# Performance work log

Measured on AMD Instinct MI355X. Metric: run time of the kernel, lower is better.

Reference implementation:

```python
import jax, jax.numpy as jnp
import numpy as np
from jax import lax

BETA = 0.95     # snn.Leaky(0.95)
THRESH = 1.0    # snntorch default threshold
ALPHA = 2.0     # snntorch ATan surrogate default alpha
NUM_STEPS = 100

@jax.custom_vjp
def spike_fn(u):
    return (u > 0).astype(u.dtype)

def _spike_fwd(u):
    return (u > 0).astype(u.dtype), u

def _spike_bwd(u, g):
    surr = (ALPHA / 2.0) / (1.0 + (jnp.pi / 2.0 * ALPHA * u) ** 2)
    return (g * surr,)

spike_fn.defvjp(_spike_fwd, _spike_bwd)

def leaky_scan(inputs, mem0):
    # inputs: [T, ...]; snntorch Leaky with reset_mechanism='zero'
    def step(carry, x_t):
        mem, _ = carry
        reset = spike_fn(mem - THRESH)       # spike detected from previous mem
        base = BETA * mem + x_t
        mem = base - reset * base            # zero-reset
        spk = spike_fn(mem - THRESH)
        return (mem, spk), None
    (mem, spk), _ = lax.scan(step, (mem0, jnp.zeros_like(mem0)), inputs)
    return spk, mem

def setup_inputs():
    key = jax.random.key(0)
    ks = jax.random.split(key, 7)
    B, T, W, C = 32, 2000, 512, 4
    H, O = 1024, 10
    s = lambda n: 1.0 / np.sqrt(n)
    return {
        "x": jax.random.normal(ks[0], (B, T, W, C), jnp.float32),
        "conv_w": jax.random.uniform(ks[1], (C,), jnp.float32, -s(C), s(C)),
        "conv_b": jax.random.uniform(ks[2], (), jnp.float32, -s(C), s(C)),
        "hidden_w": jax.random.uniform(ks[3], (H, W), jnp.float32, -s(W), s(W)),
        "hidden_b": jax.random.uniform(ks[4], (H,), jnp.float32, -s(W), s(W)),
        "out_w": jax.random.uniform(ks[5], (O, H), jnp.float32, -s(H), s(H)),
        "out_b": jax.random.uniform(ks[6], (O,), jnp.float32, -s(H), s(H)),
    }

def reference(x, conv_w, conv_b, hidden_w, hidden_b, out_w, out_b):
    B, T, W, _ = x.shape
    # 1x1 conv fusing 4 antenna channels: (B,T,W,4)->(B,T,W)
    fused = jnp.einsum('bhwc,c->bhw', x, conv_w) + conv_b
    G = T // NUM_STEPS
    fused = fused.reshape(B, G, NUM_STEPS, W)      # [B,G,S,W]
    seq1 = jnp.moveaxis(fused, 2, 0)               # [S,B,G,W] time-major
    spk, _ = leaky_scan(seq1, jnp.zeros((B, G, W), x.dtype))
    hidden = spk @ hidden_w.T + hidden_b           # [B,G,H]
    seq2 = jnp.moveaxis(hidden, 1, 0)              # [G,B,H]
    spk2, _ = leaky_scan(seq2, jnp.zeros((B, hidden.shape[2]), x.dtype))
    out = spk2 @ out_w.T + out_b                   # [B,O]
    return jax.nn.softmax(out, axis=1)
```

## Files before the change

kernel.cpp:

```cpp
#include <hip/hip_runtime.h>
#include <hip/hip_bf16.h>

typedef float f32x4 __attribute__((ext_vector_type(4)));

#define NB 32
#define NT 2000
#define NW 512
#define NG 20
#define NS 100
#define NH 1024
#define NO 10
#define BETA 0.95f
#define THRESH 1.0f

__global__ __launch_bounds__(256) void k1_conv_scan_tr(
    const f32x4* __restrict__ x,
    const float* __restrict__ cw,
    const float* __restrict__ cb,
    float* __restrict__ spk1,
    const float* __restrict__ wsrc,
    float* __restrict__ wT)
{
    __shared__ float tile[32][33];
    int bid = blockIdx.x;

    if (bid < 1280) {
        int half = bid & 1;
        int bg = bid >> 1;
        int g = bg % NG;
        int b = bg / NG;
        int tid = threadIdx.x;

        const f32x4* __restrict__ base =
            x + ((size_t)(b * NT + g * NS) * NW + half * 256);

        float w0 = cw[0], w1 = cw[1], w2 = cw[2], w3 = cw[3];
        float bias = cb[0];

        f32x4 A[10], B[10];
        float mem = 0.0f;

#define LOAD10(dst, S0)                                                        \
    {                                                                          \
        _Pragma("unroll")                                                      \
        for (int j = 0; j < 10; ++j)                                           \
            dst[j] = __builtin_nontemporal_load(base + (tid + ((S0) + j) * NW)); \
    }
#define STEP10(src)                                                            \
    {                                                                          \
        _Pragma("unroll")                                                      \
        for (int j = 0; j < 10; ++j) {                                         \
            f32x4 v = src[j];                                                  \
            float f = fmaf(v[0], w0, fmaf(v[1], w1,                            \
                      fmaf(v[2], w2, fmaf(v[3], w3, bias))));                  \
            float base_m = fmaf(BETA, mem, f);                                 \
            mem = (mem > THRESH) ? 0.0f : base_m;                              \
        }                                                                      \
    }

        LOAD10(A, 0)
        LOAD10(B, 10) STEP10(A)
        LOAD10(A, 20) STEP10(B)
        LOAD10(B, 30) STEP10(A)
        LOAD10(A, 40) STEP10(B)
        LOAD10(B, 50) STEP10(A)
        LOAD10(A, 60) STEP10(B)
        LOAD10(B, 70) STEP10(A)
        LOAD10(A, 80) STEP10(B)
        LOAD10(B, 90) STEP10(A)
        STEP10(B)
#undef LOAD10
#undef STEP10

        spk1[(b * NG + g) * NW + half * 256 + tid] = (mem > THRESH) ? 1.0f : 0.0f;
    } else {
        int tbid = bid - 1280;
        int bk = tbid & 15;
        int bh = tbid >> 4;
        int tx = threadIdx.x & 31;
        int ty = threadIdx.x >> 5;
        #pragma unroll
        for (int j = 0; j < 4; ++j)
            tile[ty + j * 8][tx] = wsrc[(bh * 32 + ty + j * 8) * NW + bk * 32 + tx];
        __syncthreads();
        #pragma unroll
        for (int j = 0; j < 4; ++j)
            wT[(bk * 32 + ty + j * 8) * NH + bh * 32 + tx] = tile[tx][ty + j * 8];
    }
}

__global__ __launch_bounds__(256) void k2_hidden_scan(
    const float* __restrict__ spk1,
    const float* __restrict__ wT,
    const float* __restrict__ hb,
    float* __restrict__ spk2)
{
    __shared__ float sk[NG][NW];
    __shared__ f32x4 red[4][10][32];

    int bid = blockIdx.x;
    int b = bid >> 3;
    int hgrp = bid & 7;
    int t = threadIdx.x;
    int lane5 = t & 31;
    int c = t >> 5;
    int h = hgrp * 128 + lane5 * 4;

    {
        const f32x4* __restrict__ sp4 =
            (const f32x4*)(spk1 + (size_t)b * NG * NW);
        f32x4* sk4 = (f32x4*)&sk[0][0];
        #pragma unroll
        for (int i = 0; i < 10; ++i)
            sk4[t + i * 256] = sp4[t + i * 256];
    }
    __syncthreads();

    f32x4 acc[NG];
    #pragma unroll
    for (int g = 0; g < NG; ++g)
        #pragma unroll
        for (int j = 0; j < 4; ++j) acc[g][j] = 0.0f;

    int k0 = c * 64;
    #pragma unroll 2
    for (int kkg = 0; kkg < 16; ++kkg) {
        int kk = k0 + kkg * 4;
        f32x4 w0 = *(const f32x4*)&wT[(kk + 0) * NH + h];
        f32x4 w1 = *(const f32x4*)&wT[(kk + 1) * NH + h];
        f32x4 w2 = *(const f32x4*)&wT[(kk + 2) * NH + h];
        f32x4 w3 = *(const f32x4*)&wT[(kk + 3) * NH + h];
        #pragma unroll
        for (int g = 0; g < NG; ++g) {
            f32x4 u = *(const f32x4*)&sk[g][kk];
            #pragma unroll
            for (int j = 0; j < 4; ++j)
                acc[g][j] = fmaf(u[0], w0[j], fmaf(u[1], w1[j],
                            fmaf(u[2], w2[j], fmaf(u[3], w3[j], acc[g][j]))));
        }
    }

    float hbias = 0.0f, mem = 0.0f;
    if (t < 128) hbias = hb[hgrp * 128 + t];
    int hl4 = t >> 2, hj = t & 3;

    #pragma unroll
    for (int half = 0; half < 2; ++half) {
        __syncthreads();
        if (c < 4) {
            #pragma unroll
            for (int gg = 0; gg < 10; ++gg)
                red[c][gg][lane5] = acc[half * 10 + gg];
        }
        __syncthreads();
        if (c >= 4) {
            #pragma unroll
            for (int gg = 0; gg < 10; ++gg) {
                f32x4 v = red[c - 4][gg][lane5];
                f32x4 a = acc[half * 10 + gg];
                #pragma unroll
                for (int j = 0; j < 4; ++j) v[j] += a[j];
                red[c - 4][gg][lane5] = v;
            }
        }
        __syncthreads();
        if (t < 128) {
            #pragma unroll
            for (int gg = 0; gg < 10; ++gg) {
                float xin = red[0][gg][hl4][hj] + red[1][gg][hl4][hj]
                          + red[2][gg][hl4][hj] + red[3][gg][hl4][hj] + hbias;
                float base = fmaf(BETA, mem, xin);
                mem = (mem > THRESH) ? 0.0f : base;
            }
        }
    }

    if (t < 128)
        spk2[b * NH + hgrp * 128 + t] = (mem > THRESH) ? 1.0f : 0.0f;
}

__global__ __launch_bounds__(256) void k3_out(
    const float* __restrict__ spk2,
    const float* __restrict__ ow,
    const float* __restrict__ ob,
    float* __restrict__ out)
{
    int b = blockIdx.x;
    int t = threadIdx.x;

    float p[NO];
    #pragma unroll
    for (int o = 0; o < NO; ++o) p[o] = 0.0f;

    for (int h = t; h < NH; h += 256) {
        float s = spk2[b * NH + h];
        #pragma unroll
        for (int o = 0; o < NO; ++o) p[o] += s * ow[o * NH + h];
    }

    __shared__ float red[NO][256];
    #pragma unroll
    for (int o = 0; o < NO; ++o) red[o][t] = p[o];
    __syncthreads();

    for (int off = 128; off > 0; off >>= 1) {
        if (t < off) {
            #pragma unroll
            for (int o = 0; o < NO; ++o) red[o][t] += red[o][t + off];
        }
        __syncthreads();
    }

    if (t == 0) {
        float v[NO], mx = -1e30f;
        #pragma unroll
        for (int o = 0; o < NO; ++o) { v[o] = red[o][0] + ob[o]; mx = fmaxf(mx, v[o]); }
        float sum = 0.0f;
        #pragma unroll
        for (int o = 0; o < NO; ++o) { v[o] = expf(v[o] - mx); sum += v[o]; }
        float inv = 1.0f / sum;
        #pragma unroll
        for (int o = 0; o < NO; ++o) out[b * NO + o] = v[o] * inv;
    }
}

extern "C" void kernel_launch(void* const* d_in, const int* in_sizes, int n_in,
                              void* d_out, int out_size, void* d_ws, size_t ws_size,
                              hipStream_t stream) {
    const f32x4*  x  = (const f32x4*)d_in[0];
    const float*  cw = (const float*)d_in[1];
    const float*  cb = (const float*)d_in[2];
    const float*  hw = (const float*)d_in[3];
    const float*  hb = (const float*)d_in[4];
    const float*  ow = (const float*)d_in[5];
    const float*  ob = (const float*)d_in[6];
    float* out = (float*)d_out;

    char* ws = (char*)d_ws;
    float* spk1 = (float*)(ws);
    float* wT   = (float*)(ws + 1310720);
    float* spk2 = (float*)(ws + 1310720 + 2097152);

    k1_conv_scan_tr<<<1792, 256, 0, stream>>>(x, cw, cb, spk1, hw, wT);

    k2_hidden_scan<<<NB * 8, 256, 0, stream>>>(spk1, wT, hb, spk2);

    k3_out<<<NB, 256, 0, stream>>>(spk2, ow, ob, out);
}
```

Measured before the change: 110.8 us.

## Fuse output projection into hidden-scan kernel and double its grid

The hidden-layer kernel now covers 64 hidden units per block instead of 128, doubling the grid to 512 blocks. It also computes per-block partial output logits with a wavefront shuffle reduction, so the spike vector no longer round-trips through memory. A tiny single-block kernel then sums the partials and applies softmax, replacing the old per-batch output kernel. The aim is better GPU occupancy in the hidden GEMM and less overhead in the tail kernel, at the cost of each block loading the spike tile into shared memory twice as often overall.

```diff
diff --git a/kernel.cpp b/kernel.cpp
--- a/kernel.cpp
+++ b/kernel.cpp
@@ -93,18 +93,19 @@
     const float* __restrict__ spk1,
     const float* __restrict__ wT,
     const float* __restrict__ hb,
-    float* __restrict__ spk2)
+    const float* __restrict__ ow,
+    float* __restrict__ partial)
 {
     __shared__ float sk[NG][NW];
-    __shared__ f32x4 red[4][10][32];
+    __shared__ float red[4][NG][64];
 
     int bid = blockIdx.x;
-    int b = bid >> 3;
-    int hgrp = bid & 7;
+    int b = bid >> 4;
+    int hgrp = bid & 15;
     int t = threadIdx.x;
     int lane5 = t & 31;
     int c = t >> 5;
-    int h = hgrp * 128 + lane5 * 4;
+    int h = hgrp * 64 + lane5 * 2;
 
     {
         const f32x4* __restrict__ sp4 =
@@ -116,111 +117,95 @@
     }
     __syncthreads();
 
-    f32x4 acc[NG];
+    float2 acc[NG];
     #pragma unroll
-    for (int g = 0; g < NG; ++g)
-        #pragma unroll
-        for (int j = 0; j < 4; ++j) acc[g][j] = 0.0f;
+    for (int g = 0; g < NG; ++g) { acc[g].x = 0.0f; acc[g].y = 0.0f; }
 
     int k0 = c * 64;
     #pragma unroll 2
     for (int kkg = 0; kkg < 16; ++kkg) {
         int kk = k0 + kkg * 4;
-        f32x4 w0 = *(const f32x4*)&wT[(kk + 0) * NH + h];
-        f32x4 w1 = *(const f32x4*)&wT[(kk + 1) * NH + h];
-        f32x4 w2 = *(const f32x4*)&wT[(kk + 2) * NH + h];
-        f32x4 w3 = *(const f32x4*)&wT[(kk + 3) * NH + h];
+        float2 a0 = *(const float2*)&wT[(kk + 0) * NH + h];
+        float2 a1 = *(const float2*)&wT[(kk + 1) * NH + h];
+        float2 a2 = *(const float2*)&wT[(kk + 2) * NH + h];
+        float2 a3 = *(const float2*)&wT[(kk + 3) * NH + h];
         #pragma unroll
         for (int g = 0; g < NG; ++g) {
             f32x4 u = *(const f32x4*)&sk[g][kk];
-            #pragma unroll
-            for (int j = 0; j < 4; ++j)
-                acc[g][j] = fmaf(u[0], w0[j], fmaf(u[1], w1[j],
-                            fmaf(u[2], w2[j], fmaf(u[3], w3[j], acc[g][j]))));
-        }
-    }
-
-    float hbias = 0.0f, mem = 0.0f;
-    if (t < 128) hbias = hb[hgrp * 128 + t];
-    int hl4 = t >> 2, hj = t & 3;
-
-    #pragma unroll
-    for (int half = 0; half < 2; ++half) {
-        __syncthreads();
-        if (c < 4) {
-            #pragma unroll
-            for (int gg = 0; gg < 10; ++gg)
-                red[c][gg][lane5] = acc[half * 10 + gg];
-        }
-        __syncthreads();
-        if (c >= 4) {
-            #pragma unroll
-            for (int gg = 0; gg < 10; ++gg) {
-                f32x4 v = red[c - 4][gg][lane5];
-                f32x4 a = acc[half * 10 + gg];
-                #pragma unroll
-                for (int j = 0; j < 4; ++j) v[j] += a[j];
-                red[c - 4][gg][lane5] = v;
-            }
-        }
-        __syncthreads();
-        if (t < 128) {
-            #pragma unroll
-            for (int gg = 0; gg < 10; ++gg) {
-                float xin = red[0][gg][hl4][hj] + red[1][gg][hl4][hj]
-                          + red[2][gg][hl4][hj] + red[3][gg][hl4][hj] + hbias;
-                float base = fmaf(BETA, mem, xin);
-                mem = (mem > THRESH) ? 0.0f : base;
-            }
-        }
-    }
-
-    if (t < 128)
-        spk2[b * NH + hgrp * 128 + t] = (mem > THRESH) ? 1.0f : 0.0f;
-}
-
-__global__ __launch_bounds__(256) void k3_out(
-    const float* __restrict__ spk2,
-    const float* __restrict__ ow,
+            acc[g].x = fmaf(u[0], a0.x, fmaf(u[1], a1.x,
+                       fmaf(u[2], a2.x, fmaf(u[3], a3.x, acc[g].x))));
+            acc[g].y = fmaf(u[0], a0.y, fmaf(u[1], a1.y,
+                       fmaf(u[2], a2.y, fmaf(u[3], a3.y, acc[g].y))));
+        }
+    }
+
+    if (c < 4) {
+        #pragma unroll
+        for (int g = 0; g < NG; ++g)
+            *(float2*)&red[c][g][lane5 * 2] = acc[g];
+    }
+    __syncthreads();
+    if (c >= 4) {
+        #pragma unroll
+        for (int g = 0; g < NG; ++g) {
+            float2 v = *(float2*)&red[c - 4][g][lane5 * 2];
+            v.x += acc[g].x; v.y += acc[g].y;
+            *(float2*)&red[c - 4][g][lane5 * 2] = v;
+        }
+    }
+    __syncthreads();
+
+    if (t < 64) {
+        float hbias = hb[hgrp * 64 + t];
+        float mem = 0.0f;
+        #pragma unroll
+        for (int g = 0; g < NG; ++g) {
+            float xin = red[0][g][t] + red[1][g][t]
+                      + red[2][g][t] + red[3][g][t] + hbias;
+            float base = fmaf(BETA, mem, xin);
+            mem = (mem > THRESH) ? 0.0f : base;
+        }
+        float spike = (mem > THRESH) ? 1.0f : 0.0f;
+
+        #pragma unroll
+        for (int o = 0; o < NO; ++o) {
+            float p = spike * ow[o * NH + hgrp * 64 + t];
+            p += __shfl_down(p, 32);
+            p += __shfl_down(p, 16);
+            p += __shfl_down(p, 8);
+            p += __shfl_down(p, 4);
+            p += __shfl_down(p, 2);
+            p += __shfl_down(p, 1);
+            if (t == 0) partial[(b * 16 + hgrp) * NO + o] = p;
+        }
+    }
+}
+
+__global__ __launch_bounds__(64) void k_softmax(
+    const float* __restrict__ partial,
     const float* __restrict__ ob,
     float* __restrict__ out)
 {
-    int b = blockIdx.x;
     int t = threadIdx.x;
-
-    float p[NO];
-    #pragma unroll
-    for (int o = 0; o < NO; ++o) p[o] = 0.0f;
-
-    for (int h = t; h < NH; h += 256) {
-        float s = spk2[b * NH + h];
-        #pragma unroll
-        for (int o = 0; o < NO; ++o) p[o] += s * ow[o * NH + h];
-    }
-
-    __shared__ float red[NO][256];
-    #pragma unroll
-    for (int o = 0; o < NO; ++o) red[o][t] = p[o];
-    __syncthreads();
-
-    for (int off = 128; off > 0; off >>= 1) {
-        if (t < off) {
+    if (t < NB) {
+        const float* p = partial + t * 16 * NO;
+        float v[NO];
+        #pragma unroll
+        for (int o = 0; o < NO; ++o) v[o] = ob[o];
+        #pragma unroll
+        for (int hg = 0; hg < 16; ++hg)
             #pragma unroll
-            for (int o = 0; o < NO; ++o) red[o][t] += red[o][t + off];
-        }
-        __syncthreads();
-    }
-
-    if (t == 0) {
-        float v[NO], mx = -1e30f;
-        #pragma unroll
-        for (int o = 0; o < NO; ++o) { v[o] = red[o][0] + ob[o]; mx = fmaxf(mx, v[o]); }
+            for (int o = 0; o < NO; ++o) v[o] += p[hg * NO + o];
+
+        float mx = -1e30f;
+        #pragma unroll
+        for (int o = 0; o < NO; ++o) mx = fmaxf(mx, v[o]);
         float sum = 0.0f;
         #pragma unroll
         for (int o = 0; o < NO; ++o) { v[o] = expf(v[o] - mx); sum += v[o]; }
         float inv = 1.0f / sum;
         #pragma unroll
-        for (int o = 0; o < NO; ++o) out[b * NO + o] = v[o] * inv;
+        for (int o = 0; o < NO; ++o) out[t * NO + o] = v[o] * inv;
     }
 }
 
@@ -237,13 +222,13 @@
     float* out = (float*)d_out;
 
     char* ws = (char*)d_ws;
-    float* spk1 = (float*)(ws);
-    float* wT   = (float*)(ws + 1310720);
-    float* spk2 = (float*)(ws + 1310720 + 2097152);
+    float* spk1    = (float*)(ws);
+    float* wT      = (float*)(ws + 1310720);
+    float* partial = (float*)(ws + 1310720 + 2097152);
 
     k1_conv_scan_tr<<<1792, 256, 0, stream>>>(x, cw, cb, spk1, hw, wT);
 
-    k2_hidden_scan<<<NB * 8, 256, 0, stream>>>(spk1, wT, hb, spk2);
-
-    k3_out<<<NB, 256, 0, stream>>>(spk2, ow, ob, out);
-}
+    k2_hidden_scan<<<NB * 16, 256, 0, stream>>>(spk1, wT, hb, ow, partial);
+
+    k_softmax<<<1, 64, 0, stream>>>(partial, ob, out);
+}
```

Measured after the change: 103.6 us, median of 2. 6.5% less time.
